# Kernel tuning notes

Measured on AMD Instinct MI355X. Metric: run time of the kernel, lower is better.

## Reference

```python
import jax, jax.numpy as jnp
import numpy as np
from jax import lax

EPS = 1e-31
V, L, B, T = 30000, 400, 16, 145
E, EH, DH, ENC, COMB = 100, 150, 200, 300, 500
SOS = 1


def setup_inputs() -> dict:
    key = jax.random.key(0)
    ks = jax.random.split(key, 32)
    def p(i, shape):
        return jax.random.normal(ks[i], shape, dtype=jnp.float32) * 0.05
    return {
        "input_tensor": jax.random.randint(ks[0], (L, B), 0, V),
        "embedding": p(1, (V, E)),
        "enc_Wih_f": p(2, (3 * EH, E)), "enc_Whh_f": p(3, (3 * EH, EH)),
        "enc_bih_f": p(4, (3 * EH,)), "enc_bhh_f": p(5, (3 * EH,)),
        "enc_Wih_b": p(6, (3 * EH, E)), "enc_Whh_b": p(7, (3 * EH, EH)),
        "enc_bih_b": p(8, (3 * EH,)), "enc_bhh_b": p(9, (3 * EH,)),
        "adapter_W": p(10, (DH, ENC)), "adapter_b": p(11, (DH,)),
        "dec_Wih": p(12, (3 * DH, E)), "dec_Whh": p(13, (3 * DH, DH)),
        "dec_bih": p(14, (3 * DH,)), "dec_bhh": p(15, (3 * DH,)),
        "bil_W": p(16, (1, DH, ENC)), "bil_b": p(17, (1,)),
        "cover_weight": jax.random.uniform(ks[18], (1,), dtype=jnp.float32),
        "ptr_W": p(19, (1, COMB)), "ptr_b": p(20, (1,)),
        "preout_W": p(21, (E, COMB)), "preout_b": p(22, (E,)),
        "out_b": p(23, (V,)),
    }


def _gru_cell(x, h, Wih, Whh, bih, bhh):
    # torch GRU cell semantics (gates ordered r, z, n)
    gi = x @ Wih.T + bih
    gh = h @ Whh.T + bhh
    ir, iz, i_n = jnp.split(gi, 3, axis=-1)
    hr, hz, hn = jnp.split(gh, 3, axis=-1)
    r = jax.nn.sigmoid(ir + hr)
    z = jax.nn.sigmoid(iz + hz)
    n = jnp.tanh(i_n + r * hn)
    return (1.0 - z) * n + z * h


def _run_gru(emb, Wih, Whh, bih, bhh):
    # emb: [L, B, E] -> outputs [L, B, H], final hidden [B, H]
    h0 = jnp.zeros((emb.shape[1], Whh.shape[1]), emb.dtype)
    def step(h, x):
        h = _gru_cell(x, h, Wih, Whh, bih, bhh)
        return h, h
    hT, ys = lax.scan(step, h0, emb)
    return ys, hT


def reference(input_tensor, embedding,
              enc_Wih_f, enc_Whh_f, enc_bih_f, enc_bhh_f,
              enc_Wih_b, enc_Whh_b, enc_bih_b, enc_bhh_b,
              adapter_W, adapter_b,
              dec_Wih, dec_Whh, dec_bih, dec_bhh,
              bil_W, bil_b, cover_weight,
              ptr_W, ptr_b, preout_W, preout_b, out_b):
    # ----- encoder: bidirectional single-layer GRU -----
    emb = embedding[input_tensor]                       # [L, B, E]
    out_f, h_f = _run_gru(emb, enc_Wih_f, enc_Whh_f, enc_bih_f, enc_bhh_f)
    out_r, h_b = _run_gru(emb[::-1], enc_Wih_b, enc_Whh_b, enc_bih_b, enc_bhh_b)
    enc_out = jnp.concatenate([out_f, out_r[::-1]], axis=-1)   # [L, B, 300]
    enc_hidden = jnp.concatenate([h_f, h_b], axis=-1)          # [B, 300]
    h0 = enc_hidden @ adapter_W.T + adapter_b                  # enc_dec_adapter -> [B, 200]

    enc_word_idx = input_tensor.T                              # [B, L]
    batch_idx = jnp.arange(enc_out.shape[1])[:, None]

    # ----- decoder: greedy loop with enc attention + coverage + pointer-gen -----
    def dec_step(carry, _):
        h, cover, tok = carry
        x = embedding[tok]                                     # [B, E]
        h = _gru_cell(x, h, dec_Wih, dec_Whh, dec_bih, dec_bhh)
        # bilinear energy: h W e + b, plus coverage term
        hW = h @ bil_W[0]                                      # [B, 300]
        energy = jnp.einsum('be,lbe->lb', hW, enc_out) + bil_b[0]
        energy = energy + cover_weight[0] * jnp.log(cover.T + EPS)
        attn = jax.nn.softmax(energy, axis=0)                  # [L, B], softmax over enc steps
        context = jnp.einsum('lbe,lb->be', enc_out, attn)      # [B, 300]
        combined = jnp.concatenate([h, context], axis=-1)      # [B, 500]
        pre = combined @ preout_W.T + preout_b                 # [B, 100]
        logits = pre @ embedding.T + out_b                     # tied output embedding [B, V]
        p_ptr = jax.nn.sigmoid(combined @ ptr_W.T + ptr_b)     # [B, 1]
        gen = jax.nn.softmax(logits, axis=1)
        attn_bl = attn.T                                       # [B, L]
        out = (1.0 - p_ptr) * gen
        out = out.at[batch_idx, enc_word_idx].add(p_ptr * attn_bl)
        new_tok = jnp.argmax(out, axis=1)
        return (h, cover + attn_bl, new_tok), out

    cover0 = jnp.zeros(enc_word_idx.shape, emb.dtype)
    tok0 = jnp.full((enc_out.shape[1],), SOS, dtype=input_tensor.dtype)
    _, outputs = lax.scan(dec_step, (h0, cover0, tok0), None, length=T)
    return outputs  # [T, B, V] pointer-generator mixture probabilities
```

## Files before the change

### kernel.cpp

```cpp
#include <hip/hip_runtime.h>

namespace {

constexpr int Vv=30000, Ll=400, Bb=16, Tt=145;
constexpr int Ee=100, EHh=150, DHh=200, ENc=300;
constexpr int SOS_TOK=1;
constexpr int NB=256, NT=512;

constexpr long SO_EMB = 0;
constexpr long SO_GIF = SO_EMB + 6400L*100;
constexpr long SO_GIB = SO_GIF + 6400L*450;
constexpr long SO_ENC = SO_GIB + 6400L*450;
constexpr long SO_WCAT= SO_GIF;

constexpr int RH    = 0;
constexpr int REXP  = 3200;
constexpr int RCTX  = 9600;
constexpr int RPREH = 22912;
constexpr int RPSUM = 24576;
constexpr int RPMAX = 28672;
constexpr int RCAND = 36864;
constexpr int RING_SZ = 49664;

constexpr long OFF_M    = 0;
constexpr long OFF_N    = OFF_M + 6400L*200;
constexpr long OFF_Q    = OFF_N + 6400L*100;
constexpr long OFF_HENC = OFF_Q + 6400;
constexpr long OFF_H0   = OFF_HENC + 4800;
constexpr long OFF_COVER= OFF_H0 + 3200;
constexpr long OFF_R143 = OFF_COVER + 8192;
constexpr long OFF_R144 = OFF_R143 + RING_SZ;
constexpr long WS_F32_END = OFF_R144 + RING_SZ;
constexpr long IWS_BYTE  = ((WS_F32_END*4 + 255)/256)*256;
constexpr int ISVL=0, IGV=6400, IGLS=12800, ICG0=19216, INGR=23328;
constexpr long BAR_BYTE  = ((IWS_BYTE + 23344L*4 + 255)/256)*256;
constexpr int HB_CNT=0, HB_GEN=32, EP_H=64, EP_CTX=96, EP_S4=128, EP_SET=160, ABRT=192;

struct Args {
  const int* itok;
  const float* emb;
  const float* Wfih; const float* Wfhh; const float* bfih; const float* bfhh;
  const float* Wbih; const float* Wbhh; const float* bbih; const float* bbhh;
  const float* adW; const float* adb;
  const float* dWih; const float* dWhh; const float* dbih; const float* dbhh;
  const float* bilW; const float* bilb; const float* cw;
  const float* ptrW; const float* ptrb;
  const float* preW; const float* preb; const float* outb;
  float* out; float* ws; int* iws; int* bar;
};

__device__ __forceinline__ int chunkStart(int c){ return c*117 + (c<48? c:48); }
__device__ __forceinline__ int chunkSize(int c){ return 117 + (c<48?1:0); }
__device__ __forceinline__ float sigm(float x){ return 1.f/(1.f+expf(-x)); }
__device__ __forceinline__ unsigned long long packvi(float val, int v){
  return ((unsigned long long)__float_as_uint(val)<<32) | (unsigned)(~(unsigned)v);
}
__device__ __forceinline__ void ast(float* p, float v){
  __hip_atomic_store(p, v, __ATOMIC_RELAXED, __HIP_MEMORY_SCOPE_AGENT); }
__device__ __forceinline__ void astu(unsigned long long* p, unsigned long long v){
  __hip_atomic_store(p, v, __ATOMIC_RELAXED, __HIP_MEMORY_SCOPE_AGENT); }
__device__ __forceinline__ int aldi(const int* p){
  return __hip_atomic_load(p, __ATOMIC_RELAXED, __HIP_MEMORY_SCOPE_AGENT); }

__device__ __forceinline__ float* ringBase(const Args& a, int t){
  if (t<=142) return a.out + (long)(t+2)*480000;
  return a.ws + (t==143 ? OFF_R143 : OFF_R144);
}

__device__ __forceinline__ void hbar(int* bar){
  __syncthreads();
  if (threadIdx.x==0){
    int* cnt=bar+HB_CNT; int* gen=bar+HB_GEN; int* abrt=bar+ABRT;
    if (aldi(abrt)==0){
      __builtin_amdgcn_fence(__ATOMIC_RELEASE, "agent");
      int g = aldi(gen);
      int arr = __hip_atomic_fetch_add(cnt, 1, __ATOMIC_RELAXED, __HIP_MEMORY_SCOPE_AGENT);
      if (arr == NB-1){
        __hip_atomic_store(cnt, 0, __ATOMIC_RELAXED, __HIP_MEMORY_SCOPE_AGENT);
        __hip_atomic_fetch_add(gen, 1, __ATOMIC_RELEASE, __HIP_MEMORY_SCOPE_AGENT);
      } else {
        long it=0;
        while (aldi(gen) == g){
          __builtin_amdgcn_s_sleep(2);
          if (++it > 2000000L){ __hip_atomic_store(abrt,1,__ATOMIC_RELAXED,__HIP_MEMORY_SCOPE_AGENT); break; }
          if ((it&1023)==0 && aldi(abrt)!=0) break;
        }
      }
      __builtin_amdgcn_fence(__ATOMIC_ACQUIRE, "agent");
    }
  }
  __syncthreads();
}

__device__ __forceinline__ void waitEp(int* ep, int target, int* abrt){
  if (threadIdx.x==0){
    if (aldi(abrt)==0){
      long it=0;
      while (aldi(ep) < target){
        if (it<32) __builtin_amdgcn_s_sleep(1); else __builtin_amdgcn_s_sleep(8);
        if (++it > 2000000L){ __hip_atomic_store(abrt,1,__ATOMIC_RELAXED,__HIP_MEMORY_SCOPE_AGENT); break; }
        if ((it&1023)==0 && aldi(abrt)!=0) break;
      }
      __builtin_amdgcn_fence(__ATOMIC_ACQUIRE, "workgroup");
    }
  }
  __syncthreads();
}
__device__ __forceinline__ void bumpEp(int* ep){
  __syncthreads();
  if (threadIdx.x==0){
    asm volatile("s_waitcnt vmcnt(0) lgkmcnt(0)" ::: "memory");
    __hip_atomic_fetch_add(ep, 1, __ATOMIC_RELAXED, __HIP_MEMORY_SCOPE_AGENT);
  }
}

__device__ void sortB(const Args& a, int b, char* smem){
  int tid=threadIdx.x;
  int* key=(int*)smem;
  key[tid] = (tid<Ll)? (a.itok[tid*16+b]*Ll + tid) : 0x7FFFFFFF;
  __syncthreads();
  for (int k=2;k<=512;k<<=1){
    for (int j=k>>1;j>0;j>>=1){
      int ixj = tid^j;
      if (ixj>tid){
        int x=key[tid], y=key[ixj];
        bool up = ((tid&k)==0);
        if ((x>y)==up){ key[tid]=y; key[ixj]=x; }
      }
      __syncthreads();
    }
  }
  int* ngS=(int*)(smem+2048);
  if (tid==0){
    int* svl=a.iws+ISVL+b*400; int* gvv=a.iws+IGV+b*400;
    int* gls=a.iws+IGLS+b*401;
    int ng=0, prev=-1;
    for (int i=0;i<400;i++){
      int kk=key[i]; int tok=kk/400, l=kk-tok*400;
      svl[i]=l;
      if (tok!=prev){ gvv[ng]=tok; gls[ng]=i; ng++; prev=tok; }
    }
    gls[ng]=400;
    a.iws[INGR+b]=ng;
    ngS[0]=ng;
  }
  __syncthreads();
  int ng=ngS[0];
  const int* gvv=a.iws+IGV+b*400;
  for (int c=tid;c<=256;c+=NT){
    int target=(c<256)? chunkStart(c) : 0x7FFFFFFF;
    int lo=0,hi=ng;
    while(lo<hi){ int mid=(lo+hi)>>1; if (gvv[mid]<target) lo=mid+1; else hi=mid; }
    a.iws[ICG0+b*257+c]=lo;
  }
}

template<int MODE>
__device__ void tileGemm(const Args& a, char* smem){
  float* Xl=(float*)smem;
  float* Wl=(float*)(smem+25600);
  const int K   = MODE? 300 : 100;
  const int NC  = MODE? 301 : 900;
  const int nCT = MODE? 5 : 15;
  const int nTiles = 100*nCT;
  const float* X = a.out + (MODE? SO_ENC : SO_EMB);
  int ty=threadIdx.x>>4, tx=threadIdx.x&15;
  for (int tile=blockIdx.x; tile<nTiles; tile+=NB){
    int rt=tile%100, ct=tile/100;
    int r0=rt*64, c0=ct*64;
    float acc[2][4];
    #pragma unroll
    for (int i=0;i<2;i++){
      #pragma unroll
      for (int j=0;j<4;j++) acc[i][j]=0.f;
    }
    for (int k0=0;k0<K;k0+=100){
      for (int i=threadIdx.x;i<1600;i+=NT){
        int rr=i/25, e4=i%25;
        ((float4*)Xl)[rr*25+e4] = *((const float4*)(X + (long)(r0+rr)*K + k0) + e4);
      }
      for (int i=threadIdx.x;i<1600;i+=NT){
        int rr=i/25, e4=i%25; int c=c0+rr;
        float4 w={0.f,0.f,0.f,0.f};
        if (c<NC){
          const float* wr;
          if (MODE==0) wr = (c<450)? (a.Wfih + (long)c*100) : (a.Wbih + (long)(c-450)*100);
          else         wr = a.out + SO_WCAT + (long)c*300 + k0;
          w = *((const float4*)wr + e4);
        }
        ((float4*)Wl)[rr*25+e4]=w;
      }
      __syncthreads();
      for (int k4=0;k4<25;k4++){
        float4 a4[2], b4[4];
        #pragma unroll
        for (int i=0;i<2;i++) a4[i]=((float4*)Xl)[(ty*2+i)*25+k4];
        #pragma unroll
        for (int j=0;j<4;j++) b4[j]=((float4*)Wl)[(tx*4+j)*25+k4];
        #pragma unroll
        for (int i=0;i<2;i++){
          #pragma unroll
          for (int j=0;j<4;j++){
            acc[i][j] += a4[i].x*b4[j].x;
            acc[i][j] += a4[i].y*b4[j].y;
            acc[i][j] += a4[i].z*b4[j].z;
            acc[i][j] += a4[i].w*b4[j].w;
          }
        }
      }
      __syncthreads();
    }
    #pragma unroll
    for (int i=0;i<2;i++){
      #pragma unroll
      for (int j=0;j<4;j++){
        int r=r0+ty*2+i, c=c0+tx*4+j;
        if (c<NC){
          if (MODE==0){
            int dir=c/450, cc=c-dir*450;
            float v=acc[i][j] + (dir? a.bbih : a.bfih)[cc];
            a.out[(dir?SO_GIB:SO_GIF) + (long)r*450 + cc]=v;
          } else {
            if (c<200)      a.ws[OFF_M + (long)r*200 + c]=acc[i][j];
            else if (c<300) a.ws[OFF_N + (long)r*100 + (c-200)]=acc[i][j];
            else            a.ws[OFF_Q + r]=acc[i][j];
          }
        }
      }
    }
  }
}

__device__ void encoderPhase(const Args& a, int bid, char* smem){
  int tid=threadIdx.x;
  int dir=bid>>4, b=bid&15;
  float* hbuf=(float*)smem;
  float* gbuf=(float*)(smem+2048);
  float* pacc=(float*)(smem+8192);
  const float* Whh = dir? a.Wbhh : a.Wfhh;
  const float* bhh = dir? a.bbhh : a.bfhh;
  const float* giBase = a.out + (dir? SO_GIB : SO_GIF);
  int ks=tid/150; int j=tid-ks*150;
  bool act = (ks<3);
  float w[3][50];
  if (act){
    #pragma unroll
    for (int g=0;g<3;g++)
      for (int k=0;k<50;k++)
        w[g][k]=Whh[(long)(g*150+j)*150 + ks*50 + k];
  }
  float b0=0,b1=0,b2=0;
  if (act && ks==0){ b0=bhh[j]; b1=bhh[150+j]; b2=bhh[300+j]; }
  for (int i=tid;i<192;i+=NT) hbuf[i]=0.f;
  {
    int l0 = dir? 399 : 0;
    for (int i=tid;i<450;i+=NT) gbuf[i]=giBase[((long)l0*16+b)*450+i];
  }
  __syncthreads();
  for (int s=0;s<400;s++){
    int p=s&1;
    int l=dir? 399-s : s;
    if (tid>=450 && s+1<400){
      int ln=dir? 399-(s+1) : s+1;
      for (int i=tid-450;i<450;i+=62) gbuf[(p^1)*452+i]=giBase[((long)ln*16+b)*450+i];
    }
    if (act){
      float ar=0.f, az=0.f, an=0.f;
      const float* hr=hbuf + p*192 + ks*64;
      #pragma unroll
      for (int k4=0;k4<12;k4++){
        float4 h4=*(const float4*)(hr + k4*4);
        ar+=h4.x*w[0][k4*4+0]; ar+=h4.y*w[0][k4*4+1]; ar+=h4.z*w[0][k4*4+2]; ar+=h4.w*w[0][k4*4+3];
        az+=h4.x*w[1][k4*4+0]; az+=h4.y*w[1][k4*4+1]; az+=h4.z*w[1][k4*4+2]; az+=h4.w*w[1][k4*4+3];
        an+=h4.x*w[2][k4*4+0]; an+=h4.y*w[2][k4*4+1]; an+=h4.z*w[2][k4*4+2]; an+=h4.w*w[2][k4*4+3];
      }
      {
        float h48=hr[48], h49=hr[49];
        ar+=h48*w[0][48]+h49*w[0][49];
        az+=h48*w[1][48]+h49*w[1][49];
        an+=h48*w[2][48]+h49*w[2][49];
      }
      pacc[(ks*3+0)*152+j]=ar;
      pacc[(ks*3+1)*152+j]=az;
      pacc[(ks*3+2)*152+j]=an;
    }
    __syncthreads();
    if (act && ks==0){
      float ar=pacc[(0*3+0)*152+j]+pacc[(1*3+0)*152+j]+pacc[(2*3+0)*152+j];
      float az=pacc[(0*3+1)*152+j]+pacc[(1*3+1)*152+j]+pacc[(2*3+1)*152+j];
      float an=pacc[(0*3+2)*152+j]+pacc[(1*3+2)*152+j]+pacc[(2*3+2)*152+j];
      const float* gi=gbuf + p*452;
      float r=sigm(gi[j]      + ar + b0);
      float z=sigm(gi[150+j]  + az + b1);
      float n=tanhf(gi[300+j] + r*(an + b2));
      int slot=(j/50)*64 + (j%50);
      float hold=hbuf[p*192+slot];
      float hv=(1.f-z)*n + z*hold;
      hbuf[(p^1)*192+slot]=hv;
      a.out[SO_ENC + ((long)l*16+b)*300 + dir*150 + j]=hv;
      if (s==399) a.ws[OFF_HENC + ((long)dir*16+b)*150 + j]=hv;
    }
    __syncthreads();
  }
}

__device__ void s1Phase(const Args& a, int bid, int t, float* slot, const float* slotP, char* smem){
  int tid=threadIdx.x;
  float* xw=(float*)smem;
  float* hw=(float*)(smem+6400);
  int* tokL=(int*)(smem+19200);
  if (t==0){
    if (tid<16) tokL[tid]=SOS_TOK;
  } else {
    const float* psum = slotP + RPSUM;
    const unsigned long long* pmax=(const unsigned long long*)(slotP + RPMAX);
    int b=tid>>5, ln=tid&31;
    float zs=0.f;
    for (int c=ln;c<256;c+=32) zs += psum[b*256+c];
    #pragma unroll
    for (int off=16;off;off>>=1) zs+=__shfl_xor(zs,off,32);
    float Z=zs;
    unsigned long long best=0;
    for (int c=ln;c<256;c+=32){
      unsigned long long pm=pmax[b*256+c];
      float ev=__uint_as_float((unsigned)(pm>>32));
      int v=(int)(~(unsigned)(pm & 0xFFFFFFFFull));
      unsigned long long pk=packvi(ev/Z, v);
      if (pk>best) best=pk;
    }
    int ng=a.iws[INGR+b];
    const float* cd=slotP + RCAND + b*800;
    const int* gvv=a.iws+IGV+b*400;
    for (int g=ln;g<ng;g+=32){
      unsigned long long pk=packvi(cd[g*2]/Z + cd[g*2+1], gvv[g]);
      if (pk>best) best=pk;
    }
    #pragma unroll
    for (int off=16;off;off>>=1){
      unsigned long long o=__shfl_xor(best,off,32);
      if (o>best) best=o;
    }
    if (ln==0) tokL[b]=(int)(~(unsigned)(best & 0xFFFFFFFFull));
  }
  __syncthreads();
  for (int i=tid;i<1600;i+=NT){ int b=i/100, e=i-b*100; xw[i]=a.emb[(long)tokL[b]*100+e]; }
  const float* hprev = (t==0)? (a.ws+OFF_H0) : (slotP+RH);
  for (int i=tid;i<3200;i+=NT) hw[i]=hprev[i];
  __syncthreads();
  {
    int pair=tid>>3, lane=tid&7;
    int uj=pair>>4, b=pair&15;
    int j=bid*4+uj;
    float air=0,aiz=0,ain=0,ahr=0,ahz=0,ahn=0;
    const float* x=xw+b*100;
    for (int k=lane;k<100;k+=8){
      float xv=x[k];
      air+=xv*a.dWih[(long)j*100+k];
      aiz+=xv*a.dWih[(long)(200+j)*100+k];
      ain+=xv*a.dWih[(long)(400+j)*100+k];
    }
    const float* h=hw+b*200;
    for (int k=lane;k<200;k+=8){
      float hv=h[k];
      ahr+=hv*a.dWhh[(long)j*200+k];
      ahz+=hv*a.dWhh[(long)(200+j)*200+k];
      ahn+=hv*a.dWhh[(long)(400+j)*200+k];
    }
    #pragma unroll
    for (int off=4;off;off>>=1){
      air+=__shfl_xor(air,off,8); aiz+=__shfl_xor(aiz,off,8); ain+=__shfl_xor(ain,off,8);
      ahr+=__shfl_xor(ahr,off,8); ahz+=__shfl_xor(ahz,off,8); ahn+=__shfl_xor(ahn,off,8);
    }
    if (lane==0){
      float r=sigm(air + a.dbih[j]     + ahr + a.dbhh[j]);
      float z=sigm(aiz + a.dbih[200+j] + ahz + a.dbhh[200+j]);
      float n=tanhf(ain + a.dbih[400+j] + r*(ahn + a.dbhh[400+j]));
      ast(slot + RH + b*200 + j, (1.f-z)*n + z*h[j]);
    }
  }
  {
    int nrows=(bid==49)?3:2;
    int unit=tid>>3, lane=tid&7;
    int jsub=unit>>4, b=unit&15;
    if (jsub<nrows){
      int j=bid*2+jsub;
      const float* w=(j<100)? (a.preW + (long)j*500) : a.ptrW;
      const float* h=hw+b*200;
      float acc=0.f;
      for (int k=lane;k<200;k+=8) acc+=h[k]*w[k];
      #pragma unroll
      for (int off=4;off;off>>=1) acc+=__shfl_xor(acc,off,8);
      if (lane==0) ast(slot + RPREH + b*104 + j, acc);
    }
  }
}

__device__ void s2ePhase(const Args& a, int idx, int t, float* slot, const float* slotP, char* smem){
  int tid=threadIdx.x;
  int b=idx&15, lg=idx>>4, l0=lg*50;
  float* hb =(float*)smem;
  float* exl=(float*)(smem+1024);
  float* zaS=(float*)(smem+1280);
  const float* hsrc=slot + RH + b*200;
  for (int i=tid;i<200;i+=NT) hb[i]=hsrc[i];
  if (tid==0){
    float za=0.f;
    if (t>0){
      #pragma unroll
      for (int g2=0;g2<8;g2++) za += slotP[RCTX + (b*8+g2)*104 + 101];
    }
    zaS[0]=za;
  }
  __syncthreads();
  int unit=tid>>3, lane=tid&7;
  if (unit<50){
    int l=l0+unit;
    const float* Mr=a.ws+OFF_M + (long)(l*16+b)*200;
    float acc=0.f;
    for (int k=lane;k<200;k+=8) acc+=hb[k]*Mr[k];
    #pragma unroll
    for (int off=4;off;off>>=1) acc+=__shfl_xor(acc,off,8);
    if (lane==0){
      float* cov=a.ws+OFF_COVER + (b*8+lg)*64 + unit;
      float cv=*cov;
      if (t>0) cv += slotP[REXP + b*400 + l] / zaS[0];
      *cov=cv;
      float en = acc + a.bilb[0] + a.cw[0]*logf(cv + 1e-31f);
      float ex = expf(en);
      ast(slot + REXP + b*400 + l, ex);
      exl[unit]=ex;
    }
  }
  __syncthreads();
  int u2=tid>>2, lane2=tid&3;
  if (u2<102){
    int k=u2; float acc=0.f;
    if (k<100){
      for (int ll=lane2;ll<50;ll+=4) acc+=exl[ll]*a.ws[OFF_N + (long)((l0+ll)*16+b)*100 + k];
    } else if (k==100){
      for (int ll=lane2;ll<50;ll+=4) acc+=exl[ll]*a.ws[OFF_Q + (l0+ll)*16 + b];
    } else {
      for (int ll=lane2;ll<50;ll+=4) acc+=exl[ll];
    }
    #pragma unroll
    for (int off=2;off;off>>=1) acc+=__shfl_xor(acc,off,4);
    if (lane2==0) ast(slot + RCTX + (b*8+lg)*104 + k, acc);
  }
}

__device__ void wbPhase(const Args& a, int c, int tr, const float* slotP, float* exPrev, char* smem){
  int tid=threadIdx.x;
  int v0=chunkStart(c), nv=chunkSize(c);
  float* zpart=(float*)(smem+8192);
  float* zl1=(float*)(smem+10240);
  float* pp1=(float*)(smem+10304);
  const float* psum = slotP + RPSUM;
  {
    int b=tid&15, seg=tid>>4;
    float z=0.f;
    for (int cc=seg;cc<256;cc+=32) z+=psum[b*256+cc];
    zpart[seg*16+b]=z;
  }
  __syncthreads();
  if (tid<16){
    int b=tid;
    float z=0.f;
    for (int s2=0;s2<32;s2++) z+=zpart[s2*16+b];
    zl1[b]=z;
    float za1=0.f, qc1=0.f;
    #pragma unroll
    for (int g2=0;g2<8;g2++){
      za1+=slotP[RCTX + (b*8+g2)*104 + 101];
      qc1+=slotP[RCTX + (b*8+g2)*104 + 100];
    }
    pp1[b]=sigm(qc1/za1 + slotP[RPREH + b*104 + 100] + a.ptrb[0]);
  }
  __syncthreads();
  if (tid<16){
    int b=tid;
    const int* cg0=a.iws+ICG0+b*257; const int* gvv=a.iws+IGV+b*400;
    const float* cd=slotP + RCAND + b*800;
    for (int g=cg0[c];g<cg0[c+1];g++){
      exPrev[(gvv[g]-v0)*17+b] += cd[g*2+1]*zl1[b];
    }
  }
  __syncthreads();
  {
    int tot=nv*16;
    for (int u=tid;u<tot;u+=NT){
      int b2=u/nv, vl=u-b2*nv;
      float sc=(1.f-pp1[b2])/zl1[b2];
      __builtin_nontemporal_store(exPrev[vl*17+b2]*sc,
                                  &a.out[((long)tr*16+b2)*30000 + v0+vl]);
    }
  }
  __syncthreads();
}

__device__ void s4Phase(const Args& a, int c, int t, float* slot, float* exCur, char* smem){
  int tid=threadIdx.x;
  int v0=chunkStart(c), nv=chunkSize(c);
  float* preL=(float*)smem;
  float* zaL =(float*)(smem+6400);
  float* ppqL=(float*)(smem+6464);
  if (tid<16){
    int b=tid;
    float za=0.f, qc=0.f;
    #pragma unroll
    for (int g2=0;g2<8;g2++){
      za+=slot[RCTX + (b*8+g2)*104 + 101];
      qc+=slot[RCTX + (b*8+g2)*104 + 100];
    }
    zaL[b]=za;
    ppqL[b]=sigm(qc/za + slot[RPREH + b*104 + 100] + a.ptrb[0]);
  }
  __syncthreads();
  for (int u=tid;u<1600;u+=NT){
    int b=u/100, k=u-b*100;
    float sv=0.f;
    #pragma unroll
    for (int g2=0;g2<8;g2++) sv+=slot[RCTX + (b*8+g2)*104 + k];
    preL[u]=sv/zaL[b] + slot[RPREH + b*104 + k] + a.preb[k];
  }
  __syncthreads();
  int bloc=tid&15;
  float4 preg[25];
  {
    const float4* p4=(const float4*)(preL + bloc*100);
    #pragma unroll
    for (int e4=0;e4<25;e4++) preg[e4]=p4[e4];
  }
  int nu=nv*16;
  const float4* emb4=(const float4*)a.emb;
  for (int u=tid;u<nu;u+=NT){
    int vl=u>>4; int v=v0+vl;
    float acc=a.outb[v];
    const float4* er=emb4 + (long)v*25;
    #pragma unroll
    for (int e4=0;e4<25;e4++){
      float4 A=er[e4], Bv=preg[e4];
      acc += A.x*Bv.x + A.y*Bv.y + A.z*Bv.z + A.w*Bv.w;
    }
    exCur[vl*17+bloc]=expf(acc);
  }
  __syncthreads();
  {
    int b=tid>>5, sg=tid&31;
    float s=0.f; unsigned long long m=0;
    for (int vl=sg;vl<nv;vl+=32){
      float ex=exCur[vl*17+b];
      s+=ex;
      unsigned long long pk=packvi(ex, v0+vl);
      if (pk>m) m=pk;
    }
    #pragma unroll
    for (int off=16;off;off>>=1){
      s+=__shfl_xor(s,off,32);
      unsigned long long om=__shfl_xor(m,off,32);
      if (om>m) m=om;
    }
    if (sg==0){
      ast(slot + RPSUM + b*256 + c, s);
      astu((unsigned long long*)(slot + RPMAX) + b*256 + c, m);
    }
  }
  if (tid<16){
    int b=tid;
    const int* cg0=a.iws+ICG0+b*257; const int* gvv=a.iws+IGV+b*400;
    const int* gls=a.iws+IGLS+b*401; const int* svl=a.iws+ISVL+b*400;
    float* cd=slot + RCAND + b*800;
    float pfac=ppqL[b]/(1.f-ppqL[b]);
    for (int g=cg0[c];g<cg0[c+1];g++){
      int v=gvv[g];
      float gs=0.f;
      for (int i2=gls[g];i2<gls[g+1];i2++) gs+=slot[REXP + b*400 + svl[i2]];
      ast(cd+g*2,   exCur[(v-v0)*17+b]);
      ast(cd+g*2+1, pfac*gs/zaL[b]);
    }
  }
}

__global__ void kInitBar(int* bar){
  int t=threadIdx.x;
  if (t<256) bar[t]=0;
}

__global__ __launch_bounds__(NT,1) void mega(Args a){
  __shared__ __align__(16) char smem[53248];
  int bid=blockIdx.x, tid=threadIdx.x;
  int* bar=a.bar;
  int* abrt=bar+ABRT;
  float* exBuf0=(float*)(smem+36864);
  float* exBuf1=(float*)(smem+44928);

  if (bid<16){
    sortB(a,bid,smem);
  } else {
    for (long i=(long)(bid-16)*NT+tid; i<640000; i+=240L*NT){
      long pair=i/100; int e=(int)(i-pair*100);
      a.out[SO_EMB+i]=a.emb[(long)a.itok[pair]*100+e];
    }
    for (int i=(bid-16)*NT+tid; i<8192; i+=240*NT) a.ws[OFF_COVER+i]=0.f;
  }
  hbar(bar);

  tileGemm<0>(a,smem);
  hbar(bar);

  if (bid<32) encoderPhase(a,bid,smem);
  hbar(bar);

  for (long i=(long)bid*NT+tid; i<90300; i+=(long)NB*NT){
    int rr=(int)(i/300), k=(int)(i-(long)rr*300);
    float v;
    if (rr<200)      v=a.bilW[(long)rr*300+k];
    else if (rr<300) v=a.preW[(long)(rr-200)*500+200+k];
    else             v=a.ptrW[200+k];
    a.out[SO_WCAT+i]=v;
  }
  if (bid>=32 && bid<48){
    int b=bid-32;
    int unit=tid>>1, lane=tid&1;
    if (unit<200){
      int j=unit;
      const float* w=a.adW+(long)j*300 + lane*150;
      const float* hh=a.ws+OFF_HENC + ((long)lane*16+b)*150;
      float acc=0.f;
      for (int e=0;e<150;e++) acc+=hh[e]*w[e];
      acc+=__shfl_xor(acc,1,2);
      if (lane==0) a.ws[OFF_H0 + b*200 + j]=acc + a.adb[j];
    }
  }
  hbar(bar);

  tileGemm<1>(a,smem);
  hbar(bar);
  bumpEp(bar+EP_SET);
  waitEp(bar+EP_SET, NB, abrt);

  for (int t=0;t<Tt;t++){
    int q=t&1;
    float* exCur  = q? exBuf1 : exBuf0;
    float* exPrev = q? exBuf0 : exBuf1;
    float* slot   = ringBase(a,t);
    float* slotP  = (t>0)? ringBase(a,t-1) : (float*)0;
    if (bid<50){
      waitEp(bar+EP_S4, 256*t, abrt);
      s1Phase(a,bid,t,slot,slotP,smem);
      bumpEp(bar+EP_H);
    } else if (bid>=64 && bid<192){
      waitEp(bar+EP_H, 50*(t+1), abrt);
      s2ePhase(a,bid-64,t,slot,slotP,smem);
      bumpEp(bar+EP_CTX);
    } else {
      waitEp(bar+EP_S4, 256*t, abrt);
    }
    if (t>0) wbPhase(a,bid,t-1,slotP,exPrev,smem);
    waitEp(bar+EP_CTX, 128*(t+1), abrt);
    s4Phase(a,bid,t,slot,exCur,smem);
    bumpEp(bar+EP_S4);
  }
  waitEp(bar+EP_S4, 256*Tt, abrt);
  wbPhase(a,bid,Tt-1,ringBase(a,Tt-1),((Tt-1)&1)?exBuf1:exBuf0,smem);
}

}

extern "C" void kernel_launch(void* const* d_in, const int* in_sizes, int n_in,
                              void* d_out, int out_size, void* d_ws, size_t ws_size,
                              hipStream_t stream) {
  Args a;
  a.itok=(const int*)d_in[0];
  a.emb =(const float*)d_in[1];
  a.Wfih=(const float*)d_in[2]; a.Wfhh=(const float*)d_in[3];
  a.bfih=(const float*)d_in[4]; a.bfhh=(const float*)d_in[5];
  a.Wbih=(const float*)d_in[6]; a.Wbhh=(const float*)d_in[7];
  a.bbih=(const float*)d_in[8]; a.bbhh=(const float*)d_in[9];
  a.adW =(const float*)d_in[10]; a.adb=(const float*)d_in[11];
  a.dWih=(const float*)d_in[12]; a.dWhh=(const float*)d_in[13];
  a.dbih=(const float*)d_in[14]; a.dbhh=(const float*)d_in[15];
  a.bilW=(const float*)d_in[16]; a.bilb=(const float*)d_in[17];
  a.cw  =(const float*)d_in[18];
  a.ptrW=(const float*)d_in[19]; a.ptrb=(const float*)d_in[20];
  a.preW=(const float*)d_in[21]; a.preb=(const float*)d_in[22];
  a.outb=(const float*)d_in[23];
  a.out =(float*)d_out;
  a.ws  =(float*)d_ws;
  a.iws =(int*)((char*)d_ws + IWS_BYTE);
  a.bar =(int*)((char*)d_ws + BAR_BYTE);

  kInitBar<<<dim3(1),dim3(256),0,stream>>>(a.bar);
  void* kargs[] = { (void*)&a };
  hipLaunchCooperativeKernel(reinterpret_cast<const void*>(mega),
                             dim3(NB), dim3(NT), kargs, 0, stream);
}
```

Baseline: 12.38 ms.

## Replace atomic counter barriers with per-block flag arrays and reorder writeback

Replaces the shared fetch-add counter barrier and epoch counters with per-block flag slots that each block stores once. A 64-lane wavefront polls the flags in parallel and checks the minimum. The change is meant to remove atomic contention on a single counter and to cut sync latency in the 145-step decoder loop. It also moves wbPhase after each block's own producer stage, so writeback overlaps with waiting, and splits the 8-way partial sums into tree adds. The cost is more polling traffic and a shorter abort timeout; correctness depends on the release/acquire fences around the flag stores being sufficient.

```diff
diff --git a/kernel.cpp b/kernel.cpp
--- a/kernel.cpp
+++ b/kernel.cpp
@@ -34,7 +34,11 @@
 constexpr long IWS_BYTE  = ((WS_F32_END*4 + 255)/256)*256;
 constexpr int ISVL=0, IGV=6400, IGLS=12800, ICG0=19216, INGR=23328;
 constexpr long BAR_BYTE  = ((IWS_BYTE + 23344L*4 + 255)/256)*256;
-constexpr int HB_CNT=0, HB_GEN=32, EP_H=64, EP_CTX=96, EP_S4=128, EP_SET=160, ABRT=192;
+constexpr int FH  =0;
+constexpr int FS1 =256;
+constexpr int FCTX=320;
+constexpr int FS4 =448;
+constexpr int ABRT=704;
 
 struct Args {
   const int* itok;
@@ -61,57 +65,49 @@
   __hip_atomic_store(p, v, __ATOMIC_RELAXED, __HIP_MEMORY_SCOPE_AGENT); }
 __device__ __forceinline__ int aldi(const int* p){
   return __hip_atomic_load(p, __ATOMIC_RELAXED, __HIP_MEMORY_SCOPE_AGENT); }
+__device__ __forceinline__ void asti(int* p, int v){
+  __hip_atomic_store(p, v, __ATOMIC_RELAXED, __HIP_MEMORY_SCOPE_AGENT); }
 
 __device__ __forceinline__ float* ringBase(const Args& a, int t){
   if (t<=142) return a.out + (long)(t+2)*480000;
   return a.ws + (t==143 ? OFF_R143 : OFF_R144);
 }
 
-__device__ __forceinline__ void hbar(int* bar){
+__device__ __forceinline__ void setFlag(int* f, int v){
+  asm volatile("s_waitcnt vmcnt(0) lgkmcnt(0)" ::: "memory");
+  __syncthreads();
+  if (threadIdx.x==0) asti(f, v);
+}
+__device__ __forceinline__ void waitFlags(const int* flags, int n, int target, int* abrt){
+  if (threadIdx.x<64){
+    int lane=threadIdx.x;
+    long it=0;
+    for (;;){
+      int mn=0x7FFFFFFF;
+      for (int i=lane;i<n;i+=64){
+        int v=aldi(flags+i);
+        if (v<mn) mn=v;
+      }
+      if (__all(mn>=target)) break;
+      __builtin_amdgcn_s_sleep(2);
+      if (++it > 400000L){ asti(abrt,1); break; }
+      if ((it&255)==0 && aldi(abrt)!=0) break;
+    }
+  }
+  __syncthreads();
+}
+
+__device__ __forceinline__ void hbarF(int* bar, int epoch){
+  asm volatile("s_waitcnt vmcnt(0) lgkmcnt(0)" ::: "memory");
   __syncthreads();
   if (threadIdx.x==0){
-    int* cnt=bar+HB_CNT; int* gen=bar+HB_GEN; int* abrt=bar+ABRT;
-    if (aldi(abrt)==0){
-      __builtin_amdgcn_fence(__ATOMIC_RELEASE, "agent");
-      int g = aldi(gen);
-      int arr = __hip_atomic_fetch_add(cnt, 1, __ATOMIC_RELAXED, __HIP_MEMORY_SCOPE_AGENT);
-      if (arr == NB-1){
-        __hip_atomic_store(cnt, 0, __ATOMIC_RELAXED, __HIP_MEMORY_SCOPE_AGENT);
-        __hip_atomic_fetch_add(gen, 1, __ATOMIC_RELEASE, __HIP_MEMORY_SCOPE_AGENT);
-      } else {
-        long it=0;
-        while (aldi(gen) == g){
-          __builtin_amdgcn_s_sleep(2);
-          if (++it > 2000000L){ __hip_atomic_store(abrt,1,__ATOMIC_RELAXED,__HIP_MEMORY_SCOPE_AGENT); break; }
-          if ((it&1023)==0 && aldi(abrt)!=0) break;
-        }
-      }
-      __builtin_amdgcn_fence(__ATOMIC_ACQUIRE, "agent");
-    }
-  }
-  __syncthreads();
-}
-
-__device__ __forceinline__ void waitEp(int* ep, int target, int* abrt){
-  if (threadIdx.x==0){
-    if (aldi(abrt)==0){
-      long it=0;
-      while (aldi(ep) < target){
-        if (it<32) __builtin_amdgcn_s_sleep(1); else __builtin_amdgcn_s_sleep(8);
-        if (++it > 2000000L){ __hip_atomic_store(abrt,1,__ATOMIC_RELAXED,__HIP_MEMORY_SCOPE_AGENT); break; }
-        if ((it&1023)==0 && aldi(abrt)!=0) break;
-      }
-      __builtin_amdgcn_fence(__ATOMIC_ACQUIRE, "workgroup");
-    }
-  }
-  __syncthreads();
-}
-__device__ __forceinline__ void bumpEp(int* ep){
-  __syncthreads();
-  if (threadIdx.x==0){
-    asm volatile("s_waitcnt vmcnt(0) lgkmcnt(0)" ::: "memory");
-    __hip_atomic_fetch_add(ep, 1, __ATOMIC_RELAXED, __HIP_MEMORY_SCOPE_AGENT);
-  }
+    __builtin_amdgcn_fence(__ATOMIC_RELEASE, "agent");
+    asti(bar+FH+blockIdx.x, epoch);
+  }
+  waitFlags(bar+FH, NB, epoch, bar+ABRT);
+  if (threadIdx.x==0)
+    __builtin_amdgcn_fence(__ATOMIC_ACQUIRE, "agent");
+  __syncthreads();
 }
 
 __device__ void sortB(const Args& a, int b, char* smem){
@@ -406,8 +402,12 @@
   if (tid==0){
     float za=0.f;
     if (t>0){
-      #pragma unroll
-      for (int g2=0;g2<8;g2++) za += slotP[RCTX + (b*8+g2)*104 + 101];
+      float s0=0,s1=0,s2=0,s3=0;
+      s0=slotP[RCTX+(b*8+0)*104+101]+slotP[RCTX+(b*8+1)*104+101];
+      s1=slotP[RCTX+(b*8+2)*104+101]+slotP[RCTX+(b*8+3)*104+101];
+      s2=slotP[RCTX+(b*8+4)*104+101]+slotP[RCTX+(b*8+5)*104+101];
+      s3=slotP[RCTX+(b*8+6)*104+101]+slotP[RCTX+(b*8+7)*104+101];
+      za=(s0+s1)+(s2+s3);
     }
     zaS[0]=za;
   }
@@ -467,13 +467,17 @@
     float z=0.f;
     for (int s2=0;s2<32;s2++) z+=zpart[s2*16+b];
     zl1[b]=z;
-    float za1=0.f, qc1=0.f;
-    #pragma unroll
-    for (int g2=0;g2<8;g2++){
-      za1+=slotP[RCTX + (b*8+g2)*104 + 101];
-      qc1+=slotP[RCTX + (b*8+g2)*104 + 100];
-    }
-    pp1[b]=sigm(qc1/za1 + slotP[RPREH + b*104 + 100] + a.ptrb[0]);
+    float za0=slotP[RCTX+(b*8+0)*104+101]+slotP[RCTX+(b*8+1)*104+101];
+    float za1=slotP[RCTX+(b*8+2)*104+101]+slotP[RCTX+(b*8+3)*104+101];
+    float za2=slotP[RCTX+(b*8+4)*104+101]+slotP[RCTX+(b*8+5)*104+101];
+    float za3=slotP[RCTX+(b*8+6)*104+101]+slotP[RCTX+(b*8+7)*104+101];
+    float qa0=slotP[RCTX+(b*8+0)*104+100]+slotP[RCTX+(b*8+1)*104+100];
+    float qa1=slotP[RCTX+(b*8+2)*104+100]+slotP[RCTX+(b*8+3)*104+100];
+    float qa2=slotP[RCTX+(b*8+4)*104+100]+slotP[RCTX+(b*8+5)*104+100];
+    float qa3=slotP[RCTX+(b*8+6)*104+100]+slotP[RCTX+(b*8+7)*104+100];
+    float za=(za0+za1)+(za2+za3);
+    float qc=(qa0+qa1)+(qa2+qa3);
+    pp1[b]=sigm(qc/za + slotP[RPREH + b*104 + 100] + a.ptrb[0]);
   }
   __syncthreads();
   if (tid<16){
@@ -505,21 +509,27 @@
   float* ppqL=(float*)(smem+6464);
   if (tid<16){
     int b=tid;
-    float za=0.f, qc=0.f;
-    #pragma unroll
-    for (int g2=0;g2<8;g2++){
-      za+=slot[RCTX + (b*8+g2)*104 + 101];
-      qc+=slot[RCTX + (b*8+g2)*104 + 100];
-    }
+    float za0=slot[RCTX+(b*8+0)*104+101]+slot[RCTX+(b*8+1)*104+101];
+    float za1=slot[RCTX+(b*8+2)*104+101]+slot[RCTX+(b*8+3)*104+101];
+    float za2=slot[RCTX+(b*8+4)*104+101]+slot[RCTX+(b*8+5)*104+101];
+    float za3=slot[RCTX+(b*8+6)*104+101]+slot[RCTX+(b*8+7)*104+101];
+    float qa0=slot[RCTX+(b*8+0)*104+100]+slot[RCTX+(b*8+1)*104+100];
+    float qa1=slot[RCTX+(b*8+2)*104+100]+slot[RCTX+(b*8+3)*104+100];
+    float qa2=slot[RCTX+(b*8+4)*104+100]+slot[RCTX+(b*8+5)*104+100];
+    float qa3=slot[RCTX+(b*8+6)*104+100]+slot[RCTX+(b*8+7)*104+100];
+    float za=(za0+za1)+(za2+za3);
+    float qc=(qa0+qa1)+(qa2+qa3);
     zaL[b]=za;
     ppqL[b]=sigm(qc/za + slot[RPREH + b*104 + 100] + a.ptrb[0]);
   }
   __syncthreads();
   for (int u=tid;u<1600;u+=NT){
     int b=u/100, k=u-b*100;
-    float sv=0.f;
-    #pragma unroll
-    for (int g2=0;g2<8;g2++) sv+=slot[RCTX + (b*8+g2)*104 + k];
+    float s0=slot[RCTX+(b*8+0)*104+k]+slot[RCTX+(b*8+1)*104+k];
+    float s1=slot[RCTX+(b*8+2)*104+k]+slot[RCTX+(b*8+3)*104+k];
+    float s2=slot[RCTX+(b*8+4)*104+k]+slot[RCTX+(b*8+5)*104+k];
+    float s3=slot[RCTX+(b*8+6)*104+k]+slot[RCTX+(b*8+7)*104+k];
+    float sv=(s0+s1)+(s2+s3);
     preL[u]=sv/zaL[b] + slot[RPREH + b*104 + k] + a.preb[k];
   }
   __syncthreads();
@@ -582,7 +592,7 @@
 
 __global__ void kInitBar(int* bar){
   int t=threadIdx.x;
-  if (t<256) bar[t]=0;
+  if (t<1024) bar[t]=0;
 }
 
 __global__ __launch_bounds__(NT,1) void mega(Args a){
@@ -602,13 +612,13 @@
     }
     for (int i=(bid-16)*NT+tid; i<8192; i+=240*NT) a.ws[OFF_COVER+i]=0.f;
   }
-  hbar(bar);
+  hbarF(bar,1);
 
   tileGemm<0>(a,smem);
-  hbar(bar);
+  hbarF(bar,2);
 
   if (bid<32) encoderPhase(a,bid,smem);
-  hbar(bar);
+  hbarF(bar,3);
 
   for (long i=(long)bid*NT+tid; i<90300; i+=(long)NB*NT){
     int rr=(int)(i/300), k=(int)(i-(long)rr*300);
@@ -631,12 +641,10 @@
       if (lane==0) a.ws[OFF_H0 + b*200 + j]=acc + a.adb[j];
     }
   }
-  hbar(bar);
+  hbarF(bar,4);
 
   tileGemm<1>(a,smem);
-  hbar(bar);
-  bumpEp(bar+EP_SET);
-  waitEp(bar+EP_SET, NB, abrt);
+  hbarF(bar,5);
 
   for (int t=0;t<Tt;t++){
     int q=t&1;
@@ -645,23 +653,27 @@
     float* slot   = ringBase(a,t);
     float* slotP  = (t>0)? ringBase(a,t-1) : (float*)0;
     if (bid<50){
-      waitEp(bar+EP_S4, 256*t, abrt);
+      if (t>0) waitFlags(bar+FS4, 256, t, abrt);
       s1Phase(a,bid,t,slot,slotP,smem);
-      bumpEp(bar+EP_H);
+      setFlag(bar+FS1+bid, t+1);
+      if (t>0) wbPhase(a,bid,t-1,slotP,exPrev,smem);
     } else if (bid>=64 && bid<192){
-      waitEp(bar+EP_H, 50*(t+1), abrt);
+      waitFlags(bar+FS1, 50, t+1, abrt);
       s2ePhase(a,bid-64,t,slot,slotP,smem);
-      bumpEp(bar+EP_CTX);
+      setFlag(bar+FCTX+(bid-64), t+1);
+      if (t>0) wbPhase(a,bid,t-1,slotP,exPrev,smem);
     } else {
-      waitEp(bar+EP_S4, 256*t, abrt);
-    }
-    if (t>0) wbPhase(a,bid,t-1,slotP,exPrev,smem);
-    waitEp(bar+EP_CTX, 128*(t+1), abrt);
+      if (t>0){
+        waitFlags(bar+FS4, 256, t, abrt);
+        wbPhase(a,bid,t-1,slotP,exPrev,smem);
+      }
+    }
+    waitFlags(bar+FCTX, 128, t+1, abrt);
     s4Phase(a,bid,t,slot,exCur,smem);
-    bumpEp(bar+EP_S4);
-  }
-  waitEp(bar+EP_S4, 256*Tt, abrt);
-  wbPhase(a,bid,Tt-1,ringBase(a,Tt-1),((Tt-1)&1)?exBuf1:exBuf0,smem);
+    setFlag(bar+FS4+bid, t+1);
+  }
+  waitFlags(bar+FS4, 256, Tt, abrt);
+  wbPhase(a,bid,Tt-1,ringBase(a,Tt-1),exBuf0,smem);
 }
 
 }
@@ -689,7 +701,7 @@
   a.iws =(int*)((char*)d_ws + IWS_BYTE);
   a.bar =(int*)((char*)d_ws + BAR_BYTE);
 
-  kInitBar<<<dim3(1),dim3(256),0,stream>>>(a.bar);
+  kInitBar<<<dim3(1),dim3(1024),0,stream>>>(a.bar);
   void* kargs[] = { (void*)&a };
   hipLaunchCooperativeKernel(reinterpret_cast<const void*>(mega),
                              dim3(NB), dim3(NT), kargs, 0, stream);
```

After: 11.34 ms. -8.4%, faster.
